# Optimization experiments

Measured on AMD Instinct MI355X. Metric: run time of the kernel, lower is better.

## Reference

```python
import jax, jax.numpy as jnp
from jax import lax
import numpy as np

B, N, C_IN = 2, 16384, 64
NPOINT, NSAMPLE = 4096, 32
RADIUS = 0.5


def setup_inputs() -> dict:
    key = jax.random.key(0)
    ks = jax.random.split(key, 8)
    xyz = jax.random.normal(ks[0], (B, N, 3), jnp.float32)
    features = jax.random.normal(ks[1], (B, C_IN, N), jnp.float32)

    def lin(k, o, i):
        return jax.random.normal(k, (o, i), jnp.float32) * (1.0 / np.sqrt(i))

    w1 = lin(ks[2], 64, C_IN + 3); b1 = jnp.zeros((64,), jnp.float32)
    w2 = lin(ks[3], 64, 64);       b2 = jnp.zeros((64,), jnp.float32)
    w3 = lin(ks[4], 128, 64);      b3 = jnp.zeros((128,), jnp.float32)
    wa = lin(ks[5], 128, 128);     ba = jnp.zeros((128,), jnp.float32)
    wc = lin(ks[6], 1, 128);       bc = jnp.zeros((1,), jnp.float32)
    return dict(xyz=xyz, features=features, w1=w1, b1=b1, w2=w2, b2=b2,
                w3=w3, b3=b3, wa=wa, ba=ba, wc=wc, bc=bc)


def farthest_point_sample(xyz, npoint):
    # d-fps: iterative furthest point sampling, seeded at index 0 (CUDA semantics)
    Bn, Nn, _ = xyz.shape

    def body(carry, _):
        dist, far = carry                                   # (B,N), (B,)
        centroid = jnp.take_along_axis(xyz, far[:, None, None], axis=1)  # (B,1,3)
        d = jnp.sum((xyz - centroid) ** 2, axis=-1)          # (B,N)
        dist = jnp.minimum(dist, d)
        nxt = jnp.argmax(dist, axis=-1).astype(jnp.int32)
        return (dist, nxt), far

    dist0 = jnp.full((Bn, Nn), 1e10, xyz.dtype)
    far0 = jnp.zeros((Bn,), jnp.int32)
    _, idx = lax.scan(body, (dist0, far0), None, length=npoint)
    return idx.T  # (B, npoint)


def ball_query(xyz, new_xyz, radius, nsample):
    # first-nsample-within-radius semantics of pointnet2 ball_query
    Nn = xyz.shape[1]
    d2 = jnp.sum((new_xyz[:, :, None, :] - xyz[:, None, :, :]) ** 2, axis=-1)  # (B,S,N)
    mask = d2 < radius * radius
    keys = jnp.where(mask, jnp.arange(Nn, dtype=jnp.int32), Nn)
    negv, _ = lax.top_k(-keys, nsample)      # nsample smallest in-ball indices
    idx = -negv                              # (B,S,nsample)
    idx_cnt = jnp.sum(mask, axis=-1)         # (B,S)
    valid = idx < Nn
    idx = jnp.where(valid, idx, idx[..., :1])          # pad with first valid idx
    idx = jnp.where(idx_cnt[..., None] > 0, idx, 0)    # empty balls -> 0 (masked later)
    return idx_cnt, idx


def reference(xyz, features, w1, b1, w2, b2, w3, b3, wa, ba, wc, bc):
    bidx = jnp.arange(B)[:, None, None]
    # sampling (d-fps) + gather
    sample_idx = farthest_point_sample(xyz, NPOINT)                    # (B,S)
    new_xyz = jnp.take_along_axis(xyz, sample_idx[..., None], axis=1)  # (B,S,3)
    # grouping (QueryAndGroup, use_xyz=True)
    idx_cnt, idx = ball_query(xyz, new_xyz, RADIUS, NSAMPLE)
    grouped_xyz = xyz[bidx, idx] - new_xyz[:, :, None, :]              # (B,S,ns,3)
    feats_t = jnp.swapaxes(features, 1, 2)                             # (B,N,C)
    grouped_feat = feats_t[bidx, idx]                                  # (B,S,ns,C)
    h = jnp.concatenate([grouped_xyz, grouped_feat], axis=-1)          # (B,S,ns,3+C)
    # shared MLP (1x1 conv + ReLU stack)
    h = jax.nn.relu(jnp.einsum('bsni,oi->bsno', h, w1) + b1)
    h = jax.nn.relu(jnp.einsum('bsni,oi->bsno', h, w2) + b2)
    h = jax.nn.relu(jnp.einsum('bsni,oi->bsno', h, w3) + b3)
    # zero empty-ball groups, then max-pool over neighbors
    h = h * (idx_cnt > 0)[:, :, None, None].astype(h.dtype)
    pooled = jnp.max(h, axis=2)                                        # (B,S,128)
    # aggregation mlp (1x1 conv1d + ReLU)
    agg = jax.nn.relu(jnp.einsum('bsi,oi->bso', pooled, wa) + ba)      # (B,S,128)
    # confidence mlp -> (B,S)
    scores = (jnp.einsum('bsi,oi->bso', agg, wc) + bc)[..., 0]
    new_features = jnp.swapaxes(agg, 1, 2)                             # (B,128,S)
    return new_xyz, new_features, scores
```

## Files before the change

### kernel.cpp

```cpp
#include <hip/hip_runtime.h>
#include <cstddef>

constexpr int kB = 2;
constexpr int kN = 16384;
constexpr int kC = 64;
constexpr int kS = 4096;
constexpr int kNS = 32;
constexpr int kNC16 = 1024;
constexpr int kNP = kN / 2;

typedef float f32x2 __attribute__((ext_vector_type(2)));

__device__ __forceinline__ unsigned expand10(unsigned v) {
  v &= 1023u;
  v = (v | (v << 16)) & 0x030000FFu;
  v = (v | (v <<  8)) & 0x0300F00Fu;
  v = (v | (v <<  4)) & 0x030C30C3u;
  v = (v | (v <<  2)) & 0x09249249u;
  return v;
}

template <int C>
__device__ __forceinline__ unsigned dpp_u32(unsigned x) {
  return (unsigned)__builtin_amdgcn_update_dpp((int)x, (int)x, C, 0xF, 0xF, false);
}
__device__ __forceinline__ unsigned max8(unsigned x) {
  x = max(x, dpp_u32<0xB1>(x));
  x = max(x, dpp_u32<0x4E>(x));
  x = max(x, dpp_u32<0x141>(x));
  return x;
}
template <int C>
__device__ __forceinline__ void u64max_dpp(unsigned& hi, unsigned& lo) {
  unsigned h2 = dpp_u32<C>(hi), l2 = dpp_u32<C>(lo);
  bool g = (h2 > hi) || (h2 == hi && l2 > lo);
  hi = g ? h2 : hi;
  lo = g ? l2 : lo;
}

#define PK_ADD(d, a, b) asm("v_pk_add_f32 %0, %1, %2" : "=v"(d) : "v"(a), "v"(b))
#define PK_MUL(d, a, b) asm("v_pk_mul_f32 %0, %1, %2" : "=v"(d) : "v"(a), "v"(b))

__global__ void transpose_kernel(const float* __restrict__ in,
                                 float* __restrict__ out,
                                 int Cdim, int Ndim) {
  __shared__ float tile[32][33];
  int b = blockIdx.z;
  int n0 = blockIdx.x * 32;
  int c0 = blockIdx.y * 32;
  int tx = threadIdx.x;
  const float* inb = in + (size_t)b * Cdim * Ndim;
  float* outb = out + (size_t)b * Cdim * Ndim;
#pragma unroll
  for (int i = threadIdx.y; i < 32; i += 8)
    tile[i][tx] = inb[(size_t)(c0 + i) * Ndim + (n0 + tx)];
  __syncthreads();
#pragma unroll
  for (int i = threadIdx.y; i < 32; i += 8)
    outb[(size_t)(n0 + i) * Cdim + (c0 + tx)] = tile[tx][i];
}

__global__ __launch_bounds__(1024) void fps_prep_kernel(
    const float* __restrict__ xyz, float* __restrict__ pxx,
    float* __restrict__ pxy, float* __restrict__ pxz,
    unsigned* __restrict__ pxo, float* __restrict__ aabb) {
  const int b = blockIdx.x;
  const int t = threadIdx.x;
  const int lane = t & 63;
  const int w = t >> 6;
  const float* P = xyz + (size_t)b * kN * 3;
  __shared__ unsigned long long keys[kN];
  __shared__ float sbb[6][16];

  float mnx = 3e38f, mny = 3e38f, mnz = 3e38f;
  float mxx = -3e38f, mxy = -3e38f, mxz = -3e38f;
  for (int p = t; p < kN; p += 1024) {
    float x = P[p * 3], y = P[p * 3 + 1], z = P[p * 3 + 2];
    mnx = fminf(mnx, x); mny = fminf(mny, y); mnz = fminf(mnz, z);
    mxx = fmaxf(mxx, x); mxy = fmaxf(mxy, y); mxz = fmaxf(mxz, z);
  }
#pragma unroll
  for (int off = 32; off >= 1; off >>= 1) {
    mnx = fminf(mnx, __shfl_xor(mnx, off, 64));
    mny = fminf(mny, __shfl_xor(mny, off, 64));
    mnz = fminf(mnz, __shfl_xor(mnz, off, 64));
    mxx = fmaxf(mxx, __shfl_xor(mxx, off, 64));
    mxy = fmaxf(mxy, __shfl_xor(mxy, off, 64));
    mxz = fmaxf(mxz, __shfl_xor(mxz, off, 64));
  }
  if (lane == 0) {
    sbb[0][w] = mnx; sbb[1][w] = mny; sbb[2][w] = mnz;
    sbb[3][w] = mxx; sbb[4][w] = mxy; sbb[5][w] = mxz;
  }
  __syncthreads();
  mnx = sbb[0][lane & 15]; mny = sbb[1][lane & 15]; mnz = sbb[2][lane & 15];
  mxx = sbb[3][lane & 15]; mxy = sbb[4][lane & 15]; mxz = sbb[5][lane & 15];
#pragma unroll
  for (int off = 8; off >= 1; off >>= 1) {
    mnx = fminf(mnx, __shfl_xor(mnx, off, 64));
    mny = fminf(mny, __shfl_xor(mny, off, 64));
    mnz = fminf(mnz, __shfl_xor(mnz, off, 64));
    mxx = fmaxf(mxx, __shfl_xor(mxx, off, 64));
    mxy = fmaxf(mxy, __shfl_xor(mxy, off, 64));
    mxz = fmaxf(mxz, __shfl_xor(mxz, off, 64));
  }
  __syncthreads();
  const float sx = 1023.0f / fmaxf(mxx - mnx, 1e-20f);
  const float sy = 1023.0f / fmaxf(mxy - mny, 1e-20f);
  const float sz = 1023.0f / fmaxf(mxz - mnz, 1e-20f);
  for (int p = t; p < kN; p += 1024) {
    float x = P[p * 3], y = P[p * 3 + 1], z = P[p * 3 + 2];
    int qx = (int)((x - mnx) * sx); qx = max(0, min(1023, qx));
    int qy = (int)((y - mny) * sy); qy = max(0, min(1023, qy));
    int qz = (int)((z - mnz) * sz); qz = max(0, min(1023, qz));
    unsigned mort = (expand10((unsigned)qx) << 2) |
                    (expand10((unsigned)qy) << 1) | expand10((unsigned)qz);
    keys[p] = ((unsigned long long)mort << 14) | (unsigned)p;
  }
  __syncthreads();
  for (unsigned k = 2; k <= (unsigned)kN; k <<= 1) {
    for (unsigned j = k >> 1; j > 0; j >>= 1) {
      for (int i = t; i < kN; i += 1024) {
        int l = i ^ (int)j;
        if (l > i) {
          unsigned long long a = keys[i], c = keys[l];
          bool asc = ((i & (int)k) == 0);
          if ((a > c) == asc) { keys[i] = c; keys[l] = a; }
        }
      }
      __syncthreads();
    }
  }
  float* FX = pxx + (size_t)b * kN;
  float* FY = pxy + (size_t)b * kN;
  float* FZ = pxz + (size_t)b * kN;
  unsigned* FO = pxo + (size_t)b * kN;
  for (int i = t; i < kN; i += 1024) {
    int o = (int)(keys[i] & 0x3FFFull);
    int c = i >> 4, j = i & 15;
    int fi = c * 16 + ((j & 7) << 1) + (j >> 3);
    FX[fi] = P[o * 3];
    FY[fi] = P[o * 3 + 1];
    FZ[fi] = P[o * 3 + 2];
    FO[fi] = 16383u - (unsigned)o;
  }
  if (t < kNC16) {
    float amn = 3e38f, bmn = 3e38f, cmn = 3e38f;
    float amx = -3e38f, bmx = -3e38f, cmx = -3e38f;
    for (int kk = 0; kk < 16; kk++) {
      int o = (int)(keys[t * 16 + kk] & 0x3FFFull);
      float x = P[o * 3], y = P[o * 3 + 1], z = P[o * 3 + 2];
      amn = fminf(amn, x); amx = fmaxf(amx, x);
      bmn = fminf(bmn, y); bmx = fmaxf(bmx, y);
      cmn = fminf(cmn, z); cmx = fmaxf(cmx, z);
    }
    float* AB = aabb + (size_t)b * 6 * kNC16;
    AB[0 * kNC16 + t] = (amn + amx) * 0.5f;
    AB[1 * kNC16 + t] = (bmn + bmx) * 0.5f;
    AB[2 * kNC16 + t] = (cmn + cmx) * 0.5f;
    AB[3 * kNC16 + t] = (amx - amn) * 0.5f * 1.0001f + 2e-7f;
    AB[4 * kNC16 + t] = (bmx - bmn) * 0.5f * 1.0001f + 2e-7f;
    AB[5 * kNC16 + t] = (cmx - cmn) * 0.5f * 1.0001f + 2e-7f;
  }
}

__global__ __launch_bounds__(1024) void fps_kernel(
    const float* __restrict__ xyz,
    const float* __restrict__ pxx, const float* __restrict__ pxy,
    const float* __restrict__ pxz, const unsigned* __restrict__ pxo,
    const float* __restrict__ aabb, float* __restrict__ new_xyz) {
  const int b = blockIdx.x;
  const int t = threadIdx.x;
  const int lane = t & 63;
  const int w = t >> 6;
  const int grp = lane >> 3;
  const int sub8 = lane & 7;
  const int s0 = (w << 6) | lane;
  const float* P = xyz + (size_t)b * kN * 3;
  const f32x2* XP = (const f32x2*)(pxx + (size_t)b * kN);
  const f32x2* YP = (const f32x2*)(pxy + (size_t)b * kN);
  const f32x2* ZP = (const f32x2*)(pxz + (size_t)b * kN);
  const uint2* OP = (const uint2*)(pxo + (size_t)b * kN);

  __shared__ f32x2 dpair[kNP];
  __shared__ uint2 M2[kNC16];
  __shared__ float4 CW[kNC16];
  __shared__ unsigned list_[16][64];
  __shared__ unsigned whi[2][16], wlo[2][16];

  for (int i = t; i < kNP; i += 1024) dpair[i] = f32x2{1e10f, 1e10f};
  if (t < kNC16) M2[t] = uint2{__float_as_uint(1e10f), 0u};

  const int c0 = (lane << 4) | w;
  const float* AB = aabb + (size_t)b * 6 * kNC16;
  float ux = AB[c0], uy = AB[kNC16 + c0], uz = AB[2 * kNC16 + c0];
  float hx = AB[3 * kNC16 + c0], hy = AB[4 * kNC16 + c0], hz = AB[5 * kNC16 + c0];
  asm volatile("" : "+v"(ux), "+v"(uy), "+v"(uz), "+v"(hx), "+v"(hy), "+v"(hz));
  __syncthreads();

  float cx = P[0], cy = P[1], cz = P[2];

  for (int it = 0; it < kS; ++it) {
    if (t == 0) {
      float* o = new_xyz + ((size_t)b * kS + it) * 3;
      o[0] = cx; o[1] = cy; o[2] = cz;
    }
    {
      float txd = fmaxf(fabsf(cx - ux) - hx, 0.0f);
      float tyd = fmaxf(fabsf(cy - uy) - hy, 0.0f);
      float tzd = fmaxf(fabsf(cz - uz) - hz, 0.0f);
      float lb2 = txd * txd + tyd * tyd + tzd * tzd;
      float Mv = __uint_as_float(M2[s0].x);
      bool fail = !(lb2 >= Mv * 1.00001f + 1e-5f);
      unsigned long long fmask = __ballot(fail);
      int nf = (int)__popcll(fmask);
      if (fail) {
        int pos = (int)__popcll(fmask & ((1ull << lane) - 1ull));
        list_[w][pos] = (unsigned)lane;
      }
      const f32x2 ncx = f32x2{-cx, -cx};
      const f32x2 ncy = f32x2{-cy, -cy};
      const f32x2 ncz = f32x2{-cz, -cz};
      const int npass = (nf + 7) >> 3;
      for (int i = 0; i < npass; ++i) {
        int idx = min(i * 8 + grp, nf - 1);
        int cl = (int)list_[w][idx];
        int pb = (((cl << 4) | w) << 3) | sub8;
        f32x2 xp = XP[pb], yp = YP[pb], zp = ZP[pb];
        uint2 op = OP[pb];
        f32x2 dold = dpair[pb];
        f32x2 dx_, dy_, dz_, xx_, yy_, zz_, s1_, d2_;
        PK_ADD(dx_, xp, ncx);
        PK_ADD(dy_, yp, ncy);
        PK_ADD(dz_, zp, ncz);
        PK_MUL(xx_, dx_, dx_);
        PK_MUL(yy_, dy_, dy_);
        PK_MUL(zz_, dz_, dz_);
        PK_ADD(s1_, xx_, yy_);
        PK_ADD(d2_, s1_, zz_);
        f32x2 dk;
        dk.x = fminf(dold.x, d2_.x);
        dk.y = fminf(dold.y, d2_.y);
        dpair[pb] = dk;
        unsigned fa = __float_as_uint(dk.x), fbv = __float_as_uint(dk.y);
        unsigned mx = max8(max(fa, fbv));
        unsigned sa = (fa == mx) ? op.x : 0u;
        unsigned sb = (fbv == mx) ? op.y : 0u;
        unsigned m2v = max8(max(sa, sb));
        const int sl = (w << 6) | cl;
        if (sub8 == 0) M2[sl] = uint2{mx, (m2v << 10) | (unsigned)sl};
        if (op.x == m2v) CW[sl] = float4{xp.x, yp.x, zp.x, 0.0f};
        if (op.y == m2v) CW[sl] = float4{xp.y, yp.y, zp.y, 0.0f};
      }
    }
    {
      uint2 m = M2[s0];
      unsigned hi = m.x, lo = m.y;
      u64max_dpp<0xB1>(hi, lo);
      u64max_dpp<0x4E>(hi, lo);
      u64max_dpp<0x124>(hi, lo);
      u64max_dpp<0x128>(hi, lo);
      u64max_dpp<0x142>(hi, lo);
      u64max_dpp<0x143>(hi, lo);
      if (lane == 63) { whi[it & 1][w] = hi; wlo[it & 1][w] = lo; }
    }
    __syncthreads();
    {
      unsigned hi = whi[it & 1][lane & 15], lo = wlo[it & 1][lane & 15];
      u64max_dpp<0x121>(hi, lo);
      u64max_dpp<0x122>(hi, lo);
      u64max_dpp<0x124>(hi, lo);
      u64max_dpp<0x128>(hi, lo);
      float4 cw = CW[lo & 1023u];
      cx = cw.x; cy = cw.y; cz = cw.z;
    }
  }
}

__global__ __launch_bounds__(256) void ball_query_kernel(const float* __restrict__ xyz,
                                                         const float* __restrict__ new_xyz,
                                                         int* __restrict__ idx) {
  const int q = (int)((blockIdx.x * 256 + threadIdx.x) >> 6);
  const int lane = threadIdx.x & 63;
  const int b = q >> 12;
  const float* P = xyz + (size_t)b * kN * 3;
  const float qx = new_xyz[q * 3 + 0];
  const float qy = new_xyz[q * 3 + 1];
  const float qz = new_xyz[q * 3 + 2];
  int cnt = 0;
  int first = -1;
  const int base = q * kNS;
  for (int j = 0; j < kN / 64; j++) {
    const int p = (j << 6) + lane;
    float dx = P[p * 3 + 0] - qx;
    float dy = P[p * 3 + 1] - qy;
    float dz = P[p * 3 + 2] - qz;
    float d = __fadd_rn(__fadd_rn(__fmul_rn(dx, dx), __fmul_rn(dy, dy)),
                        __fmul_rn(dz, dz));
    bool inb = d < 0.25f;
    unsigned long long m = __ballot(inb);
    if (first < 0 && m != 0ull) first = (j << 6) + (__ffsll(m) - 1);
    if (inb && cnt < kNS) {
      int r = cnt + (int)__popcll(m & ((1ull << lane) - 1ull));
      if (r < kNS) idx[base + r] = p;
    }
    cnt += (int)__popcll(m);
    if (cnt >= kNS) break;
  }
  if (cnt < kNS) {
    int fill = (first >= 0) ? first : 0;
    if (lane >= cnt && lane < kNS) idx[base + lane] = fill;
  }
}

__global__ __launch_bounds__(128) void group_mlp_kernel(
    const float* __restrict__ xyz, const float* __restrict__ new_xyz,
    const float* __restrict__ featsT, const int* __restrict__ nidx,
    const float* __restrict__ w1, const float* __restrict__ b1,
    const float* __restrict__ w2, const float* __restrict__ b2,
    const float* __restrict__ w3, const float* __restrict__ b3,
    const float* __restrict__ wa, const float* __restrict__ ba,
    const float* __restrict__ wc, const float* __restrict__ bc,
    float* __restrict__ aggT, float* __restrict__ scores) {
  __shared__ float smem[2 * 4384];
  const int wid = threadIdx.x >> 6;
  const int lane = threadIdx.x & 63;
  const int q = blockIdx.x * 2 + wid;
  const int b = q >> 12;
  float* Xs = smem + wid * 4384;
  float* H1 = Xs + 32 * 68;
  float* pool = H1 + 32 * 64;
  int* idxs = (int*)(pool + 128);

  if (lane < 32) idxs[lane] = nidx[q * kNS + lane];
  const float qx = new_xyz[q * 3 + 0];
  const float qy = new_xyz[q * 3 + 1];
  const float qz = new_xyz[q * 3 + 2];
  __syncthreads();

  const float* P = xyz + (size_t)b * kN * 3;
  const float* F = featsT + (size_t)b * kN * kC;
  if (lane < 32) {
    int p = idxs[lane];
    Xs[lane * 68 + 0] = P[p * 3 + 0] - qx;
    Xs[lane * 68 + 1] = P[p * 3 + 1] - qy;
    Xs[lane * 68 + 2] = P[p * 3 + 2] - qz;
  } else {
    Xs[(lane - 32) * 68 + 67] = 0.0f;
  }
  for (int j = 0; j < 32; j++) {
    Xs[j * 68 + 3 + lane] = F[(size_t)idxs[j] * kC + lane];
  }
  __syncthreads();

  float w[68];
  {
    const int o = lane;
#pragma unroll
    for (int k = 0; k < 67; k++) w[k] = w1[o * 67 + k];
    w[67] = 0.0f;
    const float bias = b1[o];
    for (int r = 0; r < 32; r++) {
      float acc = bias;
#pragma unroll
      for (int k4 = 0; k4 < 17; k4++) {
        float4 x = *(const float4*)&Xs[r * 68 + k4 * 4];
        acc += x.x * w[k4 * 4 + 0] + x.y * w[k4 * 4 + 1] +
               x.z * w[k4 * 4 + 2] + x.w * w[k4 * 4 + 3];
      }
      H1[r * 64 + o] = fmaxf(acc, 0.0f);
    }
  }
  __syncthreads();
  {
    const int o = lane;
#pragma unroll
    for (int k = 0; k < 64; k++) w[k] = w2[o * 64 + k];
    const float bias = b2[o];
    for (int r = 0; r < 32; r++) {
      float acc = bias;
#pragma unroll
      for (int k4 = 0; k4 < 16; k4++) {
        float4 x = *(const float4*)&H1[r * 64 + k4 * 4];
        acc += x.x * w[k4 * 4 + 0] + x.y * w[k4 * 4 + 1] +
               x.z * w[k4 * 4 + 2] + x.w * w[k4 * 4 + 3];
      }
      Xs[r * 64 + o] = fmaxf(acc, 0.0f);
    }
  }
  __syncthreads();
  {
    const int c = lane;
    float wB[64];
#pragma unroll
    for (int k = 0; k < 64; k++) {
      w[k] = w3[c * 64 + k];
      wB[k] = w3[(c + 64) * 64 + k];
    }
    const float biasA = b3[c];
    const float biasB = b3[c + 64];
    float pa = 0.0f, pb = 0.0f;
    for (int r = 0; r < 32; r++) {
      float a = biasA, bb = biasB;
#pragma unroll
      for (int k4 = 0; k4 < 16; k4++) {
        float4 x = *(const float4*)&Xs[r * 64 + k4 * 4];
        a  += x.x * w[k4 * 4 + 0] + x.y * w[k4 * 4 + 1] +
              x.z * w[k4 * 4 + 2] + x.w * w[k4 * 4 + 3];
        bb += x.x * wB[k4 * 4 + 0] + x.y * wB[k4 * 4 + 1] +
              x.z * wB[k4 * 4 + 2] + x.w * wB[k4 * 4 + 3];
      }
      pa = fmaxf(pa, a);
      pb = fmaxf(pb, bb);
    }
    pool[c] = pa;
    pool[c + 64] = pb;
  }
  __syncthreads();
  {
    const int c = lane;
    float accA = ba[c], accB = ba[c + 64];
#pragma unroll
    for (int k4 = 0; k4 < 32; k4++) {
      float4 pv = *(const float4*)&pool[k4 * 4];
      float4 wva = *(const float4*)&wa[c * 128 + k4 * 4];
      float4 wvb = *(const float4*)&wa[(c + 64) * 128 + k4 * 4];
      accA += pv.x * wva.x + pv.y * wva.y + pv.z * wva.z + pv.w * wva.w;
      accB += pv.x * wvb.x + pv.y * wvb.y + pv.z * wvb.z + pv.w * wvb.w;
    }
    float aggA = fmaxf(accA, 0.0f);
    float aggB = fmaxf(accB, 0.0f);
    aggT[(size_t)q * 128 + c] = aggA;
    aggT[(size_t)q * 128 + 64 + c] = aggB;
    float partial = aggA * wc[c] + aggB * wc[c + 64];
#pragma unroll
    for (int off = 32; off >= 1; off >>= 1) partial += __shfl_xor(partial, off, 64);
    if (lane == 0) scores[q] = partial + bc[0];
  }
}

extern "C" void kernel_launch(void* const* d_in, const int* in_sizes, int n_in,
                              void* d_out, int out_size, void* d_ws, size_t ws_size,
                              hipStream_t stream) {
  const float* xyz   = (const float*)d_in[0];
  const float* feats = (const float*)d_in[1];
  const float* w1 = (const float*)d_in[2];
  const float* b1 = (const float*)d_in[3];
  const float* w2 = (const float*)d_in[4];
  const float* b2 = (const float*)d_in[5];
  const float* w3 = (const float*)d_in[6];
  const float* b3 = (const float*)d_in[7];
  const float* wa = (const float*)d_in[8];
  const float* ba = (const float*)d_in[9];
  const float* wc = (const float*)d_in[10];
  const float* bc = (const float*)d_in[11];

  float* out_new_xyz = (float*)d_out;
  float* out_feat    = out_new_xyz + (size_t)kB * kS * 3;
  float* out_scores  = out_feat + (size_t)kB * 128 * kS;

  char* ws = (char*)d_ws;
  float* featsT = (float*)ws;
  int*   idxbuf = (int*)(ws + (size_t)8 * 1024 * 1024);
  float* aggT   = (float*)(ws + (size_t)9 * 1024 * 1024);
  float*    pxx = (float*)(ws + (size_t)9 * 1024 * 1024);
  float*    pxy = (float*)(ws + (size_t)9 * 1024 * 1024 + 128 * 1024);
  float*    pxz = (float*)(ws + (size_t)9 * 1024 * 1024 + 256 * 1024);
  unsigned* pxo = (unsigned*)(ws + (size_t)9 * 1024 * 1024 + 384 * 1024);
  float*   aabb = (float*)(ws + (size_t)9 * 1024 * 1024 + 512 * 1024);

  transpose_kernel<<<dim3(kN / 32, kC / 32, kB), dim3(32, 8, 1), 0, stream>>>(
      feats, featsT, kC, kN);
  fps_prep_kernel<<<dim3(kB), dim3(1024), 0, stream>>>(
      xyz, pxx, pxy, pxz, pxo, aabb);
  fps_kernel<<<dim3(kB), dim3(1024), 0, stream>>>(
      xyz, pxx, pxy, pxz, pxo, aabb, out_new_xyz);
  ball_query_kernel<<<dim3(kB * kS / 4), dim3(256), 0, stream>>>(
      xyz, out_new_xyz, idxbuf);
  group_mlp_kernel<<<dim3(kB * kS / 2), dim3(128), 0, stream>>>(
      xyz, out_new_xyz, featsT, idxbuf,
      w1, b1, w2, b2, w3, b3, wa, ba, wc, bc, aggT, out_scores);
  transpose_kernel<<<dim3(128 / 32, kS / 32, kB), dim3(32, 8, 1), 0, stream>>>(
      aggT, out_feat, kS, 128);
}
```

Before: 6.138 ms.

## Fuse FPS, ball query and MLP into persistent kernel with progress flags

Merges the FPS, ball-query, grouped MLP and output transpose into one persistent kernel. Two blocks run FPS and publish progress through global atomic counters every 32 samples. The other 254 blocks spin-wait on those counters and process each query's ball query and MLP as soon as its centroid exists, writing out_feat in transposed layout directly. This is meant to hide the ball-query and MLP work behind the serial FPS loop and remove the intermediate idx and aggT buffers. It relies on all 256 blocks being co-resident and uses a bounded spin guard, so correctness depends on the scheduler.

```diff
diff --git a/kernel.cpp b/kernel.cpp
--- a/kernel.cpp
+++ b/kernel.cpp
@@ -63,11 +63,14 @@
 __global__ __launch_bounds__(1024) void fps_prep_kernel(
     const float* __restrict__ xyz, float* __restrict__ pxx,
     float* __restrict__ pxy, float* __restrict__ pxz,
-    unsigned* __restrict__ pxo, float* __restrict__ aabb) {
+    unsigned* __restrict__ pxo, float* __restrict__ aabb,
+    unsigned* __restrict__ prog) {
   const int b = blockIdx.x;
   const int t = threadIdx.x;
   const int lane = t & 63;
   const int w = t >> 6;
+  if (t == 0)
+    __hip_atomic_store(&prog[b], 0u, __ATOMIC_RELEASE, __HIP_MEMORY_SCOPE_AGENT);
   const float* P = xyz + (size_t)b * kN * 3;
   __shared__ unsigned long long keys[kN];
   __shared__ float sbb[6][16];
@@ -164,278 +167,268 @@
   }
 }
 
-__global__ __launch_bounds__(1024) void fps_kernel(
+__global__ __launch_bounds__(1024) void fused_kernel(
     const float* __restrict__ xyz,
     const float* __restrict__ pxx, const float* __restrict__ pxy,
     const float* __restrict__ pxz, const unsigned* __restrict__ pxo,
-    const float* __restrict__ aabb, float* __restrict__ new_xyz) {
-  const int b = blockIdx.x;
-  const int t = threadIdx.x;
-  const int lane = t & 63;
-  const int w = t >> 6;
-  const int grp = lane >> 3;
-  const int sub8 = lane & 7;
-  const int s0 = (w << 6) | lane;
-  const float* P = xyz + (size_t)b * kN * 3;
-  const f32x2* XP = (const f32x2*)(pxx + (size_t)b * kN);
-  const f32x2* YP = (const f32x2*)(pxy + (size_t)b * kN);
-  const f32x2* ZP = (const f32x2*)(pxz + (size_t)b * kN);
-  const uint2* OP = (const uint2*)(pxo + (size_t)b * kN);
-
-  __shared__ f32x2 dpair[kNP];
-  __shared__ uint2 M2[kNC16];
-  __shared__ float4 CW[kNC16];
-  __shared__ unsigned list_[16][64];
-  __shared__ unsigned whi[2][16], wlo[2][16];
-
-  for (int i = t; i < kNP; i += 1024) dpair[i] = f32x2{1e10f, 1e10f};
-  if (t < kNC16) M2[t] = uint2{__float_as_uint(1e10f), 0u};
-
-  const int c0 = (lane << 4) | w;
-  const float* AB = aabb + (size_t)b * 6 * kNC16;
-  float ux = AB[c0], uy = AB[kNC16 + c0], uz = AB[2 * kNC16 + c0];
-  float hx = AB[3 * kNC16 + c0], hy = AB[4 * kNC16 + c0], hz = AB[5 * kNC16 + c0];
-  asm volatile("" : "+v"(ux), "+v"(uy), "+v"(uz), "+v"(hx), "+v"(hy), "+v"(hz));
-  __syncthreads();
-
-  float cx = P[0], cy = P[1], cz = P[2];
-
-  for (int it = 0; it < kS; ++it) {
-    if (t == 0) {
-      float* o = new_xyz + ((size_t)b * kS + it) * 3;
-      o[0] = cx; o[1] = cy; o[2] = cz;
-    }
-    {
-      float txd = fmaxf(fabsf(cx - ux) - hx, 0.0f);
-      float tyd = fmaxf(fabsf(cy - uy) - hy, 0.0f);
-      float tzd = fmaxf(fabsf(cz - uz) - hz, 0.0f);
-      float lb2 = txd * txd + tyd * tyd + tzd * tzd;
-      float Mv = __uint_as_float(M2[s0].x);
-      bool fail = !(lb2 >= Mv * 1.00001f + 1e-5f);
-      unsigned long long fmask = __ballot(fail);
-      int nf = (int)__popcll(fmask);
-      if (fail) {
-        int pos = (int)__popcll(fmask & ((1ull << lane) - 1ull));
-        list_[w][pos] = (unsigned)lane;
-      }
-      const f32x2 ncx = f32x2{-cx, -cx};
-      const f32x2 ncy = f32x2{-cy, -cy};
-      const f32x2 ncz = f32x2{-cz, -cz};
-      const int npass = (nf + 7) >> 3;
-      for (int i = 0; i < npass; ++i) {
-        int idx = min(i * 8 + grp, nf - 1);
-        int cl = (int)list_[w][idx];
-        int pb = (((cl << 4) | w) << 3) | sub8;
-        f32x2 xp = XP[pb], yp = YP[pb], zp = ZP[pb];
-        uint2 op = OP[pb];
-        f32x2 dold = dpair[pb];
-        f32x2 dx_, dy_, dz_, xx_, yy_, zz_, s1_, d2_;
-        PK_ADD(dx_, xp, ncx);
-        PK_ADD(dy_, yp, ncy);
-        PK_ADD(dz_, zp, ncz);
-        PK_MUL(xx_, dx_, dx_);
-        PK_MUL(yy_, dy_, dy_);
-        PK_MUL(zz_, dz_, dz_);
-        PK_ADD(s1_, xx_, yy_);
-        PK_ADD(d2_, s1_, zz_);
-        f32x2 dk;
-        dk.x = fminf(dold.x, d2_.x);
-        dk.y = fminf(dold.y, d2_.y);
-        dpair[pb] = dk;
-        unsigned fa = __float_as_uint(dk.x), fbv = __float_as_uint(dk.y);
-        unsigned mx = max8(max(fa, fbv));
-        unsigned sa = (fa == mx) ? op.x : 0u;
-        unsigned sb = (fbv == mx) ? op.y : 0u;
-        unsigned m2v = max8(max(sa, sb));
-        const int sl = (w << 6) | cl;
-        if (sub8 == 0) M2[sl] = uint2{mx, (m2v << 10) | (unsigned)sl};
-        if (op.x == m2v) CW[sl] = float4{xp.x, yp.x, zp.x, 0.0f};
-        if (op.y == m2v) CW[sl] = float4{xp.y, yp.y, zp.y, 0.0f};
-      }
-    }
-    {
-      uint2 m = M2[s0];
-      unsigned hi = m.x, lo = m.y;
-      u64max_dpp<0xB1>(hi, lo);
-      u64max_dpp<0x4E>(hi, lo);
-      u64max_dpp<0x124>(hi, lo);
-      u64max_dpp<0x128>(hi, lo);
-      u64max_dpp<0x142>(hi, lo);
-      u64max_dpp<0x143>(hi, lo);
-      if (lane == 63) { whi[it & 1][w] = hi; wlo[it & 1][w] = lo; }
-    }
-    __syncthreads();
-    {
-      unsigned hi = whi[it & 1][lane & 15], lo = wlo[it & 1][lane & 15];
-      u64max_dpp<0x121>(hi, lo);
-      u64max_dpp<0x122>(hi, lo);
-      u64max_dpp<0x124>(hi, lo);
-      u64max_dpp<0x128>(hi, lo);
-      float4 cw = CW[lo & 1023u];
-      cx = cw.x; cy = cw.y; cz = cw.z;
-    }
-  }
-}
-
-__global__ __launch_bounds__(256) void ball_query_kernel(const float* __restrict__ xyz,
-                                                         const float* __restrict__ new_xyz,
-                                                         int* __restrict__ idx) {
-  const int q = (int)((blockIdx.x * 256 + threadIdx.x) >> 6);
-  const int lane = threadIdx.x & 63;
-  const int b = q >> 12;
-  const float* P = xyz + (size_t)b * kN * 3;
-  const float qx = new_xyz[q * 3 + 0];
-  const float qy = new_xyz[q * 3 + 1];
-  const float qz = new_xyz[q * 3 + 2];
-  int cnt = 0;
-  int first = -1;
-  const int base = q * kNS;
-  for (int j = 0; j < kN / 64; j++) {
-    const int p = (j << 6) + lane;
-    float dx = P[p * 3 + 0] - qx;
-    float dy = P[p * 3 + 1] - qy;
-    float dz = P[p * 3 + 2] - qz;
-    float d = __fadd_rn(__fadd_rn(__fmul_rn(dx, dx), __fmul_rn(dy, dy)),
-                        __fmul_rn(dz, dz));
-    bool inb = d < 0.25f;
-    unsigned long long m = __ballot(inb);
-    if (first < 0 && m != 0ull) first = (j << 6) + (__ffsll(m) - 1);
-    if (inb && cnt < kNS) {
-      int r = cnt + (int)__popcll(m & ((1ull << lane) - 1ull));
-      if (r < kNS) idx[base + r] = p;
-    }
-    cnt += (int)__popcll(m);
-    if (cnt >= kNS) break;
-  }
-  if (cnt < kNS) {
-    int fill = (first >= 0) ? first : 0;
-    if (lane >= cnt && lane < kNS) idx[base + lane] = fill;
-  }
-}
-
-__global__ __launch_bounds__(128) void group_mlp_kernel(
-    const float* __restrict__ xyz, const float* __restrict__ new_xyz,
-    const float* __restrict__ featsT, const int* __restrict__ nidx,
+    const float* __restrict__ aabb, const float* __restrict__ featsT,
     const float* __restrict__ w1, const float* __restrict__ b1,
     const float* __restrict__ w2, const float* __restrict__ b2,
     const float* __restrict__ w3, const float* __restrict__ b3,
     const float* __restrict__ wa, const float* __restrict__ ba,
     const float* __restrict__ wc, const float* __restrict__ bc,
-    float* __restrict__ aggT, float* __restrict__ scores) {
-  __shared__ float smem[2 * 4384];
-  const int wid = threadIdx.x >> 6;
-  const int lane = threadIdx.x & 63;
-  const int q = blockIdx.x * 2 + wid;
-  const int b = q >> 12;
-  float* Xs = smem + wid * 4384;
-  float* H1 = Xs + 32 * 68;
-  float* pool = H1 + 32 * 64;
-  int* idxs = (int*)(pool + 128);
-
-  if (lane < 32) idxs[lane] = nidx[q * kNS + lane];
-  const float qx = new_xyz[q * 3 + 0];
-  const float qy = new_xyz[q * 3 + 1];
-  const float qz = new_xyz[q * 3 + 2];
-  __syncthreads();
-
-  const float* P = xyz + (size_t)b * kN * 3;
-  const float* F = featsT + (size_t)b * kN * kC;
-  if (lane < 32) {
-    int p = idxs[lane];
-    Xs[lane * 68 + 0] = P[p * 3 + 0] - qx;
-    Xs[lane * 68 + 1] = P[p * 3 + 1] - qy;
-    Xs[lane * 68 + 2] = P[p * 3 + 2] - qz;
+    float* __restrict__ new_xyz, float* __restrict__ out_feat,
+    float* __restrict__ scores, unsigned* __restrict__ prog) {
+  __shared__ __align__(16) char smem[16 * 8832];
+  const int blk = blockIdx.x;
+  const int t = threadIdx.x;
+  const int lane = t & 63;
+  const int w = t >> 6;
+
+  if (blk < 2) {
+    const int bb = blk;
+    const int grp = lane >> 3;
+    const int sub8 = lane & 7;
+    const int s0 = (w << 6) | lane;
+    const float* P = xyz + (size_t)bb * kN * 3;
+    const f32x2* XP = (const f32x2*)(pxx + (size_t)bb * kN);
+    const f32x2* YP = (const f32x2*)(pxy + (size_t)bb * kN);
+    const f32x2* ZP = (const f32x2*)(pxz + (size_t)bb * kN);
+    const uint2* OP = (const uint2*)(pxo + (size_t)bb * kN);
+
+    float4* CW = (float4*)smem;
+    f32x2* dpair = (f32x2*)(smem + 16384);
+    uint2* M2 = (uint2*)(smem + 81920);
+    unsigned* list_ = (unsigned*)(smem + 90112);
+    unsigned* whi = (unsigned*)(smem + 94208);
+    unsigned* wlo = whi + 32;
+
+    for (int i = t; i < kNP; i += 1024) dpair[i] = f32x2{1e10f, 1e10f};
+    if (t < kNC16) M2[t] = uint2{__float_as_uint(1e10f), 0u};
+
+    const int c0 = (lane << 4) | w;
+    const float* AB = aabb + (size_t)bb * 6 * kNC16;
+    float ux = AB[c0], uy = AB[kNC16 + c0], uz = AB[2 * kNC16 + c0];
+    float hx = AB[3 * kNC16 + c0], hy = AB[4 * kNC16 + c0], hz = AB[5 * kNC16 + c0];
+    asm volatile("" : "+v"(ux), "+v"(uy), "+v"(uz), "+v"(hx), "+v"(hy), "+v"(hz));
+    __syncthreads();
+
+    float cx = P[0], cy = P[1], cz = P[2];
+
+    for (int it = 0; it < kS; ++it) {
+      if (t == 0) {
+        float* o = new_xyz + ((size_t)bb * kS + it) * 3;
+        o[0] = cx; o[1] = cy; o[2] = cz;
+        if (((it + 1) & 31) == 0)
+          __hip_atomic_store(&prog[bb], (unsigned)(it + 1),
+                             __ATOMIC_RELEASE, __HIP_MEMORY_SCOPE_AGENT);
+      }
+      {
+        float txd = fmaxf(fabsf(cx - ux) - hx, 0.0f);
+        float tyd = fmaxf(fabsf(cy - uy) - hy, 0.0f);
+        float tzd = fmaxf(fabsf(cz - uz) - hz, 0.0f);
+        float lb2 = txd * txd + tyd * tyd + tzd * tzd;
+        float Mv = __uint_as_float(M2[s0].x);
+        bool fail = !(lb2 >= Mv * 1.00001f + 1e-5f);
+        unsigned long long fmask = __ballot(fail);
+        int nf = (int)__popcll(fmask);
+        if (fail) {
+          int pos = (int)__popcll(fmask & ((1ull << lane) - 1ull));
+          list_[w * 64 + pos] = (unsigned)lane;
+        }
+        const f32x2 ncx = f32x2{-cx, -cx};
+        const f32x2 ncy = f32x2{-cy, -cy};
+        const f32x2 ncz = f32x2{-cz, -cz};
+        const int npass = (nf + 7) >> 3;
+        for (int i = 0; i < npass; ++i) {
+          int idx = min(i * 8 + grp, nf - 1);
+          int cl = (int)list_[w * 64 + idx];
+          int pb = (((cl << 4) | w) << 3) | sub8;
+          f32x2 xp = XP[pb], yp = YP[pb], zp = ZP[pb];
+          uint2 op = OP[pb];
+          f32x2 dold = dpair[pb];
+          f32x2 dx_, dy_, dz_, xx_, yy_, zz_, s1_, d2_;
+          PK_ADD(dx_, xp, ncx);
+          PK_ADD(dy_, yp, ncy);
+          PK_ADD(dz_, zp, ncz);
+          PK_MUL(xx_, dx_, dx_);
+          PK_MUL(yy_, dy_, dy_);
+          PK_MUL(zz_, dz_, dz_);
+          PK_ADD(s1_, xx_, yy_);
+          PK_ADD(d2_, s1_, zz_);
+          f32x2 dk;
+          dk.x = fminf(dold.x, d2_.x);
+          dk.y = fminf(dold.y, d2_.y);
+          dpair[pb] = dk;
+          unsigned fa = __float_as_uint(dk.x), fbv = __float_as_uint(dk.y);
+          unsigned mx = max8(max(fa, fbv));
+          unsigned sa = (fa == mx) ? op.x : 0u;
+          unsigned sb = (fbv == mx) ? op.y : 0u;
+          unsigned m2v = max8(max(sa, sb));
+          const int sl = (w << 6) | cl;
+          if (sub8 == 0) M2[sl] = uint2{mx, (m2v << 10) | (unsigned)sl};
+          if (op.x == m2v) CW[sl] = float4{xp.x, yp.x, zp.x, 0.0f};
+          if (op.y == m2v) CW[sl] = float4{xp.y, yp.y, zp.y, 0.0f};
+        }
+      }
+      {
+        uint2 m = M2[s0];
+        unsigned hi = m.x, lo = m.y;
+        u64max_dpp<0xB1>(hi, lo);
+        u64max_dpp<0x4E>(hi, lo);
+        u64max_dpp<0x124>(hi, lo);
+        u64max_dpp<0x128>(hi, lo);
+        u64max_dpp<0x142>(hi, lo);
+        u64max_dpp<0x143>(hi, lo);
+        if (lane == 63) { whi[(it & 1) * 16 + w] = hi; wlo[(it & 1) * 16 + w] = lo; }
+      }
+      __syncthreads();
+      {
+        unsigned hi = whi[(it & 1) * 16 + (lane & 15)];
+        unsigned lo = wlo[(it & 1) * 16 + (lane & 15)];
+        u64max_dpp<0x121>(hi, lo);
+        u64max_dpp<0x122>(hi, lo);
+        u64max_dpp<0x124>(hi, lo);
+        u64max_dpp<0x128>(hi, lo);
+        float4 cw = CW[lo & 1023u];
+        cx = cw.x; cy = cw.y; cz = cw.z;
+      }
+    }
+    if (t == 0)
+      __hip_atomic_store(&prog[bb], (unsigned)kS,
+                         __ATOMIC_RELEASE, __HIP_MEMORY_SCOPE_AGENT);
   } else {
-    Xs[(lane - 32) * 68 + 67] = 0.0f;
-  }
-  for (int j = 0; j < 32; j++) {
-    Xs[j * 68 + 3 + lane] = F[(size_t)idxs[j] * kC + lane];
-  }
-  __syncthreads();
-
-  float w[68];
-  {
-    const int o = lane;
-#pragma unroll
-    for (int k = 0; k < 67; k++) w[k] = w1[o * 67 + k];
-    w[67] = 0.0f;
-    const float bias = b1[o];
-    for (int r = 0; r < 32; r++) {
-      float acc = bias;
-#pragma unroll
-      for (int k4 = 0; k4 < 17; k4++) {
-        float4 x = *(const float4*)&Xs[r * 68 + k4 * 4];
-        acc += x.x * w[k4 * 4 + 0] + x.y * w[k4 * 4 + 1] +
-               x.z * w[k4 * 4 + 2] + x.w * w[k4 * 4 + 3];
-      }
-      H1[r * 64 + o] = fmaxf(acc, 0.0f);
+    float* Xs = (float*)(smem + (size_t)w * 8832);
+    int* idxs = (int*)(Xs + 32 * 68);
+    const int v = (blk - 2) * 16 + w;
+    for (int g = v; g < kB * kS; g += 4064) {
+      const int b = g >> 12;
+      const int q = g & (kS - 1);
+      const unsigned tgt = (unsigned)q + 1u;
+      int guard = 0;
+      while (__hip_atomic_load(&prog[b], __ATOMIC_ACQUIRE,
+                               __HIP_MEMORY_SCOPE_AGENT) < tgt &&
+             guard < (1 << 21)) {
+        __builtin_amdgcn_s_sleep(32);
+        ++guard;
+      }
+      const float* nxp = new_xyz + ((size_t)b * kS + q) * 3;
+      const float qx = __hip_atomic_load(nxp + 0, __ATOMIC_RELAXED, __HIP_MEMORY_SCOPE_AGENT);
+      const float qy = __hip_atomic_load(nxp + 1, __ATOMIC_RELAXED, __HIP_MEMORY_SCOPE_AGENT);
+      const float qz = __hip_atomic_load(nxp + 2, __ATOMIC_RELAXED, __HIP_MEMORY_SCOPE_AGENT);
+      const float* Pb = xyz + (size_t)b * kN * 3;
+      const float* F = featsT + (size_t)b * kN * kC;
+      {
+        int cnt = 0;
+        int first = -1;
+        for (int j = 0; j < kN / 64; j++) {
+          const int p = (j << 6) + lane;
+          float dx = Pb[p * 3 + 0] - qx;
+          float dy = Pb[p * 3 + 1] - qy;
+          float dz = Pb[p * 3 + 2] - qz;
+          float d = __fadd_rn(__fadd_rn(__fmul_rn(dx, dx), __fmul_rn(dy, dy)),
+                              __fmul_rn(dz, dz));
+          bool inb = d < 0.25f;
+          unsigned long long m = __ballot(inb);
+          if (first < 0 && m != 0ull) first = (j << 6) + (__ffsll(m) - 1);
+          if (inb && cnt < kNS) {
+            int r = cnt + (int)__popcll(m & ((1ull << lane) - 1ull));
+            if (r < kNS) idxs[r] = p;
+          }
+          cnt += (int)__popcll(m);
+          if (cnt >= kNS) break;
+        }
+        if (cnt < kNS) {
+          int fill = (first >= 0) ? first : 0;
+          if (lane >= cnt && lane < kNS) idxs[lane] = fill;
+        }
+      }
+      if (lane < 32) {
+        int p = idxs[lane];
+        Xs[lane * 68 + 0] = Pb[p * 3 + 0] - qx;
+        Xs[lane * 68 + 1] = Pb[p * 3 + 1] - qy;
+        Xs[lane * 68 + 2] = Pb[p * 3 + 2] - qz;
+      } else {
+        Xs[(lane - 32) * 68 + 67] = 0.0f;
+      }
+      for (int j = 0; j < 32; j++)
+        Xs[j * 68 + 3 + lane] = F[(size_t)idxs[j] * kC + lane];
+      {
+        float wv[68];
+#pragma unroll
+        for (int k = 0; k < 67; k++) wv[k] = w1[lane * 67 + k];
+        wv[67] = 0.0f;
+        const float bias = b1[lane];
+        for (int r = 0; r < 32; r++) {
+          float acc = bias;
+#pragma unroll
+          for (int k4 = 0; k4 < 17; k4++) {
+            float4 x = *(const float4*)&Xs[r * 68 + k4 * 4];
+            acc += x.x * wv[k4 * 4 + 0] + x.y * wv[k4 * 4 + 1] +
+                   x.z * wv[k4 * 4 + 2] + x.w * wv[k4 * 4 + 3];
+          }
+          Xs[r * 68 + lane] = fmaxf(acc, 0.0f);
+        }
+      }
+      {
+        float wv[64];
+#pragma unroll
+        for (int k = 0; k < 64; k++) wv[k] = w2[lane * 64 + k];
+        const float bias = b2[lane];
+        for (int r = 0; r < 32; r++) {
+          float acc = bias;
+#pragma unroll
+          for (int k4 = 0; k4 < 16; k4++) {
+            float4 x = *(const float4*)&Xs[r * 68 + k4 * 4];
+            acc += x.x * wv[k4 * 4 + 0] + x.y * wv[k4 * 4 + 1] +
+                   x.z * wv[k4 * 4 + 2] + x.w * wv[k4 * 4 + 3];
+          }
+          Xs[r * 68 + lane] = fmaxf(acc, 0.0f);
+        }
+      }
+      float pph[2];
+#pragma unroll
+      for (int h = 0; h < 2; h++) {
+        float wv[64];
+#pragma unroll
+        for (int k = 0; k < 64; k++) wv[k] = w3[(lane + 64 * h) * 64 + k];
+        const float bias = b3[lane + 64 * h];
+        float pm = 0.0f;
+        for (int r = 0; r < 32; r++) {
+          float acc = bias;
+#pragma unroll
+          for (int k4 = 0; k4 < 16; k4++) {
+            float4 x = *(const float4*)&Xs[r * 68 + k4 * 4];
+            acc += x.x * wv[k4 * 4 + 0] + x.y * wv[k4 * 4 + 1] +
+                   x.z * wv[k4 * 4 + 2] + x.w * wv[k4 * 4 + 3];
+          }
+          pm = fmaxf(pm, acc);
+        }
+        pph[h] = pm;
+      }
+      Xs[lane] = pph[0];
+      Xs[64 + lane] = pph[1];
+      {
+        float accA = ba[lane], accB = ba[lane + 64];
+#pragma unroll
+        for (int k4 = 0; k4 < 32; k4++) {
+          float4 pv = *(const float4*)&Xs[k4 * 4];
+          float4 wva = *(const float4*)&wa[lane * 128 + k4 * 4];
+          float4 wvb = *(const float4*)&wa[(lane + 64) * 128 + k4 * 4];
+          accA += pv.x * wva.x + pv.y * wva.y + pv.z * wva.z + pv.w * wva.w;
+          accB += pv.x * wvb.x + pv.y * wvb.y + pv.z * wvb.z + pv.w * wvb.w;
+        }
+        float aggA = fmaxf(accA, 0.0f);
+        float aggB = fmaxf(accB, 0.0f);
+        out_feat[((size_t)b * 128 + lane) * kS + q] = aggA;
+        out_feat[((size_t)b * 128 + 64 + lane) * kS + q] = aggB;
+        float partial = aggA * wc[lane] + aggB * wc[lane + 64];
+#pragma unroll
+        for (int off = 32; off >= 1; off >>= 1)
+          partial += __shfl_xor(partial, off, 64);
+        if (lane == 0) scores[(size_t)b * kS + q] = partial + bc[0];
+      }
     }
-  }
-  __syncthreads();
-  {
-    const int o = lane;
-#pragma unroll
-    for (int k = 0; k < 64; k++) w[k] = w2[o * 64 + k];
-    const float bias = b2[o];
-    for (int r = 0; r < 32; r++) {
-      float acc = bias;
-#pragma unroll
-      for (int k4 = 0; k4 < 16; k4++) {
-        float4 x = *(const float4*)&H1[r * 64 + k4 * 4];
-        acc += x.x * w[k4 * 4 + 0] + x.y * w[k4 * 4 + 1] +
-               x.z * w[k4 * 4 + 2] + x.w * w[k4 * 4 + 3];
-      }
-      Xs[r * 64 + o] = fmaxf(acc, 0.0f);
-    }
-  }
-  __syncthreads();
-  {
-    const int c = lane;
-    float wB[64];
-#pragma unroll
-    for (int k = 0; k < 64; k++) {
-      w[k] = w3[c * 64 + k];
-      wB[k] = w3[(c + 64) * 64 + k];
-    }
-    const float biasA = b3[c];
-    const float biasB = b3[c + 64];
-    float pa = 0.0f, pb = 0.0f;
-    for (int r = 0; r < 32; r++) {
-      float a = biasA, bb = biasB;
-#pragma unroll
-      for (int k4 = 0; k4 < 16; k4++) {
-        float4 x = *(const float4*)&Xs[r * 64 + k4 * 4];
-        a  += x.x * w[k4 * 4 + 0] + x.y * w[k4 * 4 + 1] +
-              x.z * w[k4 * 4 + 2] + x.w * w[k4 * 4 + 3];
-        bb += x.x * wB[k4 * 4 + 0] + x.y * wB[k4 * 4 + 1] +
-              x.z * wB[k4 * 4 + 2] + x.w * wB[k4 * 4 + 3];
-      }
-      pa = fmaxf(pa, a);
-      pb = fmaxf(pb, bb);
-    }
-    pool[c] = pa;
-    pool[c + 64] = pb;
-  }
-  __syncthreads();
-  {
-    const int c = lane;
-    float accA = ba[c], accB = ba[c + 64];
-#pragma unroll
-    for (int k4 = 0; k4 < 32; k4++) {
-      float4 pv = *(const float4*)&pool[k4 * 4];
-      float4 wva = *(const float4*)&wa[c * 128 + k4 * 4];
-      float4 wvb = *(const float4*)&wa[(c + 64) * 128 + k4 * 4];
-      accA += pv.x * wva.x + pv.y * wva.y + pv.z * wva.z + pv.w * wva.w;
-      accB += pv.x * wvb.x + pv.y * wvb.y + pv.z * wvb.z + pv.w * wvb.w;
-    }
-    float aggA = fmaxf(accA, 0.0f);
-    float aggB = fmaxf(accB, 0.0f);
-    aggT[(size_t)q * 128 + c] = aggA;
-    aggT[(size_t)q * 128 + 64 + c] = aggB;
-    float partial = aggA * wc[c] + aggB * wc[c + 64];
-#pragma unroll
-    for (int off = 32; off >= 1; off >>= 1) partial += __shfl_xor(partial, off, 64);
-    if (lane == 0) scores[q] = partial + bc[0];
   }
 }
 
@@ -461,25 +454,19 @@
 
   char* ws = (char*)d_ws;
   float* featsT = (float*)ws;
-  int*   idxbuf = (int*)(ws + (size_t)8 * 1024 * 1024);
-  float* aggT   = (float*)(ws + (size_t)9 * 1024 * 1024);
   float*    pxx = (float*)(ws + (size_t)9 * 1024 * 1024);
   float*    pxy = (float*)(ws + (size_t)9 * 1024 * 1024 + 128 * 1024);
   float*    pxz = (float*)(ws + (size_t)9 * 1024 * 1024 + 256 * 1024);
   unsigned* pxo = (unsigned*)(ws + (size_t)9 * 1024 * 1024 + 384 * 1024);
   float*   aabb = (float*)(ws + (size_t)9 * 1024 * 1024 + 512 * 1024);
+  unsigned* prog = (unsigned*)(ws + (size_t)9 * 1024 * 1024 + 576 * 1024);
 
   transpose_kernel<<<dim3(kN / 32, kC / 32, kB), dim3(32, 8, 1), 0, stream>>>(
       feats, featsT, kC, kN);
   fps_prep_kernel<<<dim3(kB), dim3(1024), 0, stream>>>(
-      xyz, pxx, pxy, pxz, pxo, aabb);
-  fps_kernel<<<dim3(kB), dim3(1024), 0, stream>>>(
-      xyz, pxx, pxy, pxz, pxo, aabb, out_new_xyz);
-  ball_query_kernel<<<dim3(kB * kS / 4), dim3(256), 0, stream>>>(
-      xyz, out_new_xyz, idxbuf);
-  group_mlp_kernel<<<dim3(kB * kS / 2), dim3(128), 0, stream>>>(
-      xyz, out_new_xyz, featsT, idxbuf,
-      w1, b1, w2, b2, w3, b3, wa, ba, wc, bc, aggT, out_scores);
-  transpose_kernel<<<dim3(128 / 32, kS / 32, kB), dim3(32, 8, 1), 0, stream>>>(
-      aggT, out_feat, kS, 128);
-}
+      xyz, pxx, pxy, pxz, pxo, aabb, prog);
+  fused_kernel<<<dim3(256), dim3(1024), 0, stream>>>(
+      xyz, pxx, pxy, pxz, pxo, aabb, featsT,
+      w1, b1, w2, b2, w3, b3, wa, ba, wc, bc,
+      out_new_xyz, out_feat, out_scores, prog);
+}
```

Measured after the change: 11.51 ms. 87.6% more time.
